# Kernel tuning notes

Measured on AMD Instinct MI355X. Metric: run time of the kernel, lower is better.

The kernel has to match this reference:

```python
import jax, jax.numpy as jnp
import numpy as np

H = 16        # query heads
HK = 8        # kv heads
D = 128       # head dim
HID = 2048    # hidden size
FF = 6144     # mlp intermediate
THETA = 1e6   # rope base (qwen3)
EPS = 1e-6
T = 2048      # total tokens


def rmsnorm(x, w):
    return x * jax.lax.rsqrt(jnp.mean(x * x, axis=-1, keepdims=True) + EPS) * w


def rope(pos, x):
    # x: [T, h, D], rotate-half RoPE
    half = D // 2
    inv = 1.0 / (THETA ** (jnp.arange(half, dtype=jnp.float32) / half))
    freqs = pos.astype(jnp.float32)[:, None] * inv          # [T, half]
    cos = jnp.cos(freqs)[:, None, :]
    sin = jnp.sin(freqs)[:, None, :]
    x1, x2 = x[..., :half], x[..., half:]
    return jnp.concatenate([x1 * cos - x2 * sin, x2 * cos + x1 * sin], axis=-1)


def setup_inputs() -> dict:
    key = jax.random.key(0)
    ks = jax.random.split(key, 12)
    s = 0.02
    return {
        "positions": jnp.arange(T, dtype=jnp.int32),
        "hidden_states": jax.random.normal(ks[0], (T, HID), dtype=jnp.float32),
        "wq": jax.random.normal(ks[1], (H * D, HID), dtype=jnp.float32) * s,
        "wk": jax.random.normal(ks[2], (HK * D, HID), dtype=jnp.float32) * s,
        "wv": jax.random.normal(ks[3], (HK * D, HID), dtype=jnp.float32) * s,
        "wo": jax.random.normal(ks[4], (HID, H * D), dtype=jnp.float32) * s,
        "q_norm_w": jnp.ones((D,), dtype=jnp.float32),
        "k_norm_w": jnp.ones((D,), dtype=jnp.float32),
        "ln1_w": jnp.ones((HID,), dtype=jnp.float32),
        "ln2_w": jnp.ones((HID,), dtype=jnp.float32),
        "w_gate": jax.random.normal(ks[5], (FF, HID), dtype=jnp.float32) * s,
        "w_up": jax.random.normal(ks[6], (FF, HID), dtype=jnp.float32) * s,
        "w_down": jax.random.normal(ks[7], (HID, FF), dtype=jnp.float32) * s,
    }


def reference(positions, hidden_states, wq, wk, wv, wo, q_norm_w, k_norm_w,
              ln1_w, ln2_w, w_gate, w_up, w_down):
    t = hidden_states.shape[0]
    residual = hidden_states
    h = rmsnorm(hidden_states, ln1_w)
    q = (h @ wq.T).reshape(t, H, D)
    k = (h @ wk.T).reshape(t, HK, D)
    v = (h @ wv.T).reshape(t, HK, D)
    q = rmsnorm(q, q_norm_w)
    k = rmsnorm(k, k_norm_w)
    q = rope(positions, q)
    k = rope(positions, k)
    # GQA: expand kv heads to query heads
    g = H // HK
    kr = jnp.repeat(k, g, axis=1)  # [t, H, D]
    vr = jnp.repeat(v, g, axis=1)
    scores = jnp.einsum('thd,shd->hts', q, kr) * (D ** -0.5)
    causal = positions[:, None] >= positions[None, :]
    scores = jnp.where(causal[None], scores, jnp.finfo(scores.dtype).min)
    p = jax.nn.softmax(scores, axis=-1)
    o = jnp.einsum('hts,shd->thd', p, vr).reshape(t, H * D)
    h = residual + o @ wo.T
    residual = h
    h = rmsnorm(h, ln2_w)
    h = (jax.nn.silu(h @ w_gate.T) * (h @ w_up.T)) @ w_down.T
    return residual + h
```

## Files before the change

kernel.cpp:

```cpp
#include <hip/hip_runtime.h>
#include <hip/hip_bf16.h>
#include <stdint.h>

namespace {

constexpr int kT   = 2048;
constexpr int kHid = 2048;
constexpr int kH   = 16;
constexpr int kHK  = 8;
constexpr int kD   = 128;
constexpr int kFF  = 6144;

using bf16x8 = __attribute__((ext_vector_type(8))) short;
using f32x4  = __attribute__((ext_vector_type(4))) float;

__device__ __forceinline__ float bf2f(unsigned short u) {
    return __uint_as_float(((unsigned)u) << 16);
}
__device__ __forceinline__ unsigned short f2bf(float f) {
    unsigned u = __float_as_uint(f);
    return (unsigned short)((u + 0x7fffu + ((u >> 16) & 1u)) >> 16);
}
__device__ __forceinline__ void gload_lds16(const void* g, void* l) {
    __builtin_amdgcn_global_load_lds(
        (__attribute__((address_space(1))) void*)g,
        (__attribute__((address_space(3))) void*)l, 16, 0, 0);
}
__device__ __forceinline__ f32x4 mf(bf16x8 a, bf16x8 b, f32x4 c) {
    return __builtin_amdgcn_mfma_f32_16x16x32_bf16(a, b, c, 0, 0, 0);
}

__global__ __launch_bounds__(256)
void cvt_f32_bf16(const float* __restrict__ src, unsigned short* __restrict__ dst, int n4) {
    int i = blockIdx.x * 256 + threadIdx.x;
    if (i < n4) {
        float4 v = ((const float4*)src)[i];
        ushort4 o;
        o.x = f2bf(v.x); o.y = f2bf(v.y); o.z = f2bf(v.z); o.w = f2bf(v.w);
        ((ushort4*)dst)[i] = o;
    }
}

__global__ __launch_bounds__(256)
void reduce4(const float* __restrict__ p0, const float* __restrict__ p1,
             const float* __restrict__ p2, const float* __restrict__ p3,
             const float* __restrict__ res, float* __restrict__ out, int n4) {
    int i = blockIdx.x * 256 + threadIdx.x;
    if (i < n4) {
        float4 a = ((const float4*)p0)[i];
        float4 b = ((const float4*)p1)[i];
        float4 c = ((const float4*)p2)[i];
        float4 d = ((const float4*)p3)[i];
        float4 r = ((const float4*)res)[i];
        float4 o;
        o.x = a.x + b.x + c.x + d.x + r.x;
        o.y = a.y + b.y + c.y + d.y + r.y;
        o.z = a.z + b.z + c.z + d.z + r.z;
        o.w = a.w + b.w + c.w + d.w + r.w;
        ((float4*)out)[i] = o;
    }
}

__global__ __launch_bounds__(256)
void rmsnorm_k(const float* __restrict__ x, const float* __restrict__ w,
               unsigned short* __restrict__ out) {
    const int row = blockIdx.x;
    const int tid = threadIdx.x;
    const float4* xr = (const float4*)(x + (size_t)row * kHid);
    float4 v0 = xr[tid];
    float4 v1 = xr[tid + 256];
    float ss = v0.x*v0.x + v0.y*v0.y + v0.z*v0.z + v0.w*v0.w
             + v1.x*v1.x + v1.y*v1.y + v1.z*v1.z + v1.w*v1.w;
#pragma unroll
    for (int m = 1; m < 64; m <<= 1) ss += __shfl_xor(ss, m);
    __shared__ float red[4];
    if ((tid & 63) == 0) red[tid >> 6] = ss;
    __syncthreads();
    float tot = red[0] + red[1] + red[2] + red[3];
    float rs = rsqrtf(tot * (1.0f / kHid) + 1e-6f);
    const float4* wv = (const float4*)w;
    float4 w0 = wv[tid], w1 = wv[tid + 256];
    ushort4 o0, o1;
    o0.x = f2bf(v0.x * rs * w0.x); o0.y = f2bf(v0.y * rs * w0.y);
    o0.z = f2bf(v0.z * rs * w0.z); o0.w = f2bf(v0.w * rs * w0.w);
    o1.x = f2bf(v1.x * rs * w1.x); o1.y = f2bf(v1.y * rs * w1.y);
    o1.z = f2bf(v1.z * rs * w1.z); o1.w = f2bf(v1.w * rs * w1.w);
    ushort4* orow = (ushort4*)(out + (size_t)row * kHid);
    orow[tid] = o0;
    orow[tid + 256] = o1;
}

__global__ __launch_bounds__(256)
void rmsnorm_red4(const float* __restrict__ p0, const float* __restrict__ p1,
                  const float* __restrict__ p2, const float* __restrict__ p3,
                  const float* __restrict__ res, const float* __restrict__ w,
                  float* __restrict__ H, unsigned short* __restrict__ out) {
    const int row = blockIdx.x;
    const int tid = threadIdx.x;
    const size_t base = (size_t)row * kHid;
    float4 v0, v1;
    {
        const float4* a = (const float4*)(p0 + base);
        const float4* b = (const float4*)(p1 + base);
        const float4* c = (const float4*)(p2 + base);
        const float4* d = (const float4*)(p3 + base);
        const float4* r = (const float4*)(res + base);
        float4 a0 = a[tid], b0 = b[tid], c0 = c[tid], d0 = d[tid], r0 = r[tid];
        v0.x = a0.x + b0.x + c0.x + d0.x + r0.x;
        v0.y = a0.y + b0.y + c0.y + d0.y + r0.y;
        v0.z = a0.z + b0.z + c0.z + d0.z + r0.z;
        v0.w = a0.w + b0.w + c0.w + d0.w + r0.w;
        float4 a1 = a[tid + 256], b1 = b[tid + 256], c1 = c[tid + 256],
               d1 = d[tid + 256], r1 = r[tid + 256];
        v1.x = a1.x + b1.x + c1.x + d1.x + r1.x;
        v1.y = a1.y + b1.y + c1.y + d1.y + r1.y;
        v1.z = a1.z + b1.z + c1.z + d1.z + r1.z;
        v1.w = a1.w + b1.w + c1.w + d1.w + r1.w;
    }
    ((float4*)(H + base))[tid] = v0;
    ((float4*)(H + base))[tid + 256] = v1;
    float ss = v0.x*v0.x + v0.y*v0.y + v0.z*v0.z + v0.w*v0.w
             + v1.x*v1.x + v1.y*v1.y + v1.z*v1.z + v1.w*v1.w;
#pragma unroll
    for (int m = 1; m < 64; m <<= 1) ss += __shfl_xor(ss, m);
    __shared__ float red[4];
    if ((tid & 63) == 0) red[tid >> 6] = ss;
    __syncthreads();
    float tot = red[0] + red[1] + red[2] + red[3];
    float rs = rsqrtf(tot * (1.0f / kHid) + 1e-6f);
    const float4* wv = (const float4*)w;
    float4 w0 = wv[tid], w1 = wv[tid + 256];
    ushort4 o0, o1;
    o0.x = f2bf(v0.x * rs * w0.x); o0.y = f2bf(v0.y * rs * w0.y);
    o0.z = f2bf(v0.z * rs * w0.z); o0.w = f2bf(v0.w * rs * w0.w);
    o1.x = f2bf(v1.x * rs * w1.x); o1.y = f2bf(v1.y * rs * w1.y);
    o1.z = f2bf(v1.z * rs * w1.z); o1.w = f2bf(v1.w * rs * w1.w);
    ushort4* orow = (ushort4*)(out + base);
    orow[tid] = o0;
    orow[tid + 256] = o1;
}

template <int EPI>
__global__ __launch_bounds__(512, 2)
void gemm256(const unsigned short* __restrict__ A,
             const unsigned short* __restrict__ B,
             void* __restrict__ C,
             int M, int N, int K, int KS,
             float* __restrict__ p0, float* __restrict__ p1,
             float* __restrict__ p2, float* __restrict__ p3) {
    __shared__ unsigned short smem[2][4][128 * 64];

    const int tid  = threadIdx.x;
    const int lane = tid & 63;
    const int l15  = lane & 15;
    const int g4   = lane >> 4;
    const int wid  = tid >> 6;
    const int wr   = wid >> 2;
    const int wc   = wid & 3;
    const int bm   = blockIdx.y * 256;
    const int bn   = blockIdx.x * 256;
    const int kb   = (EPI == 4) ? blockIdx.z * KS : 0;
    const int NT   = ((EPI == 4) ? KS : K) >> 6;
    const int NI   = NT >> 1;

    f32x4 acc[8][4] = {};

    auto stage = [&](int b, int reg, int t) {
        const unsigned short* Base = (reg < 2) ? A : B;
        const int br = ((reg < 2) ? bm : bn) + (reg & 1) * 128;
#pragma unroll
        for (int i = 0; i < 2; ++i) {
            int ch   = tid + i * 512;
            int row  = ch >> 3;
            int slot = (ch & 7) ^ (row & 7);
            gload_lds16(Base + (size_t)(br + row) * K + kb + t * 64 + slot * 8,
                        (char*)&smem[b][reg][0] + ch * 16);
        }
    };
    auto rdA = [&](int b, int m, int ks) {
        int row = m * 16 + l15;
        return *(const bf16x8*)((const char*)&smem[b][wr][0]
               + row * 128 + (((ks * 4 + g4) ^ (row & 7)) * 16));
    };
    auto rdB = [&](int b, int n, int ks) {
        int row = wc * 64 + n * 16 + l15;
        return *(const bf16x8*)((const char*)&smem[b][2 + (row >> 7)][0]
               + (row & 127) * 128 + (((ks * 4 + g4) ^ (row & 7)) * 16));
    };

    stage(0, 2, 0); stage(0, 3, 0); stage(0, 0, 0); stage(0, 1, 0);
    stage(1, 2, 1); stage(1, 3, 1); stage(1, 0, 1);
    asm volatile("s_waitcnt vmcnt(6)" ::: "memory");
    __builtin_amdgcn_s_barrier();

    for (int i = 0; i < NI; ++i) {
        const int e  = 2 * i;
        const int o  = e + 1;
        const bool pf = (e + 2 < NT);
        bf16x8 af[4][2], bfr[4][2];

#pragma unroll
        for (int m = 0; m < 4; ++m) { af[m][0] = rdA(0, m, 0); af[m][1] = rdA(0, m, 1); }
#pragma unroll
        for (int n = 0; n < 4; ++n) { bfr[n][0] = rdB(0, n, 0); bfr[n][1] = rdB(0, n, 1); }
        stage(1, 1, o);
        __builtin_amdgcn_s_barrier();
        asm volatile("s_waitcnt lgkmcnt(0)" ::: "memory");
        __builtin_amdgcn_sched_barrier(0);
        __builtin_amdgcn_s_setprio(1);
#pragma unroll
        for (int m = 0; m < 4; ++m)
#pragma unroll
            for (int n = 0; n < 2; ++n) {
                acc[m][n] = mf(af[m][0], bfr[n][0], acc[m][n]);
                acc[m][n] = mf(af[m][1], bfr[n][1], acc[m][n]);
            }
        __builtin_amdgcn_s_setprio(0);
        __builtin_amdgcn_s_barrier();

        if (pf) stage(0, 2, e + 2);
        __builtin_amdgcn_s_barrier();
        __builtin_amdgcn_s_setprio(1);
#pragma unroll
        for (int m = 0; m < 4; ++m)
#pragma unroll
            for (int n = 2; n < 4; ++n) {
                acc[m][n] = mf(af[m][0], bfr[n][0], acc[m][n]);
                acc[m][n] = mf(af[m][1], bfr[n][1], acc[m][n]);
            }
        __builtin_amdgcn_s_setprio(0);
        __builtin_amdgcn_s_barrier();

#pragma unroll
        for (int m = 0; m < 4; ++m) { af[m][0] = rdA(0, 4 + m, 0); af[m][1] = rdA(0, 4 + m, 1); }
        if (pf) stage(0, 3, e + 2);
        __builtin_amdgcn_s_barrier();
        asm volatile("s_waitcnt lgkmcnt(0)" ::: "memory");
        __builtin_amdgcn_sched_barrier(0);
        __builtin_amdgcn_s_setprio(1);
#pragma unroll
        for (int m = 0; m < 4; ++m)
#pragma unroll
            for (int n = 0; n < 2; ++n) {
                acc[4 + m][n] = mf(af[m][0], bfr[n][0], acc[4 + m][n]);
                acc[4 + m][n] = mf(af[m][1], bfr[n][1], acc[4 + m][n]);
            }
        __builtin_amdgcn_s_setprio(0);
        __builtin_amdgcn_s_barrier();

        if (pf) stage(0, 0, e + 2);
        __builtin_amdgcn_s_barrier();
        __builtin_amdgcn_s_setprio(1);
#pragma unroll
        for (int m = 0; m < 4; ++m)
#pragma unroll
            for (int n = 2; n < 4; ++n) {
                acc[4 + m][n] = mf(af[m][0], bfr[n][0], acc[4 + m][n]);
                acc[4 + m][n] = mf(af[m][1], bfr[n][1], acc[4 + m][n]);
            }
        __builtin_amdgcn_s_setprio(0);
        if (pf) asm volatile("s_waitcnt vmcnt(6)" ::: "memory");
        else    asm volatile("s_waitcnt vmcnt(0)" ::: "memory");
        __builtin_amdgcn_s_barrier();

#pragma unroll
        for (int m = 0; m < 4; ++m) { af[m][0] = rdA(1, m, 0); af[m][1] = rdA(1, m, 1); }
#pragma unroll
        for (int n = 0; n < 4; ++n) { bfr[n][0] = rdB(1, n, 0); bfr[n][1] = rdB(1, n, 1); }
        if (pf) stage(0, 1, e + 2);
        __builtin_amdgcn_s_barrier();
        asm volatile("s_waitcnt lgkmcnt(0)" ::: "memory");
        __builtin_amdgcn_sched_barrier(0);
        __builtin_amdgcn_s_setprio(1);
#pragma unroll
        for (int m = 0; m < 4; ++m)
#pragma unroll
            for (int n = 0; n < 2; ++n) {
                acc[m][n] = mf(af[m][0], bfr[n][0], acc[m][n]);
                acc[m][n] = mf(af[m][1], bfr[n][1], acc[m][n]);
            }
        __builtin_amdgcn_s_setprio(0);
        __builtin_amdgcn_s_barrier();

        if (pf) stage(1, 2, o + 2);
        __builtin_amdgcn_s_barrier();
        __builtin_amdgcn_s_setprio(1);
#pragma unroll
        for (int m = 0; m < 4; ++m)
#pragma unroll
            for (int n = 2; n < 4; ++n) {
                acc[m][n] = mf(af[m][0], bfr[n][0], acc[m][n]);
                acc[m][n] = mf(af[m][1], bfr[n][1], acc[m][n]);
            }
        __builtin_amdgcn_s_setprio(0);
        __builtin_amdgcn_s_barrier();

#pragma unroll
        for (int m = 0; m < 4; ++m) { af[m][0] = rdA(1, 4 + m, 0); af[m][1] = rdA(1, 4 + m, 1); }
        if (pf) stage(1, 3, o + 2);
        __builtin_amdgcn_s_barrier();
        asm volatile("s_waitcnt lgkmcnt(0)" ::: "memory");
        __builtin_amdgcn_sched_barrier(0);
        __builtin_amdgcn_s_setprio(1);
#pragma unroll
        for (int m = 0; m < 4; ++m)
#pragma unroll
            for (int n = 0; n < 2; ++n) {
                acc[4 + m][n] = mf(af[m][0], bfr[n][0], acc[4 + m][n]);
                acc[4 + m][n] = mf(af[m][1], bfr[n][1], acc[4 + m][n]);
            }
        __builtin_amdgcn_s_setprio(0);
        __builtin_amdgcn_s_barrier();

        if (pf) stage(1, 0, o + 2);
        __builtin_amdgcn_s_barrier();
        __builtin_amdgcn_s_setprio(1);
#pragma unroll
        for (int m = 0; m < 4; ++m)
#pragma unroll
            for (int n = 2; n < 4; ++n) {
                acc[4 + m][n] = mf(af[m][0], bfr[n][0], acc[4 + m][n]);
                acc[4 + m][n] = mf(af[m][1], bfr[n][1], acc[4 + m][n]);
            }
        __builtin_amdgcn_s_setprio(0);
        if (pf) asm volatile("s_waitcnt vmcnt(6)" ::: "memory");
        __builtin_amdgcn_s_barrier();
    }

    float* P = nullptr;
    if (EPI == 4) {
        const int z = blockIdx.z;
        P = (z == 0) ? p0 : (z == 1) ? p1 : (z == 2) ? p2 : p3;
    }
#pragma unroll
    for (int m = 0; m < 8; ++m) {
#pragma unroll
        for (int n = 0; n < 4; ++n) {
            int row = bm + wr * 128 + m * 16 + g4 * 4;
            int col = bn + wc * 64 + n * 16 + l15;
#pragma unroll
            for (int r = 0; r < 4; ++r) {
                size_t idx = (size_t)(row + r) * N + col;
                float v = acc[m][n][r];
                if (EPI == 0) ((float*)C)[idx] = v;
                else          P[idx] = v;
            }
        }
    }
}

template <int EPI>
__global__ __launch_bounds__(512, 2)
void gemm128(const unsigned short* __restrict__ A,
             const unsigned short* __restrict__ B,
             void* __restrict__ C,
             int M, int N, int K, int KS,
             float* __restrict__ p0, float* __restrict__ p1) {
    __shared__ unsigned short smem[2][3][128 * 64];

    const int tid  = threadIdx.x;
    const int lane = tid & 63;
    const int l15  = lane & 15;
    const int g4   = lane >> 4;
    const int wid  = tid >> 6;
    const int wr   = wid >> 2;
    const int wc   = wid & 3;
    const int bm   = blockIdx.y * 128;
    const int bn   = blockIdx.x * 256;
    const int kb   = (EPI == 4) ? blockIdx.z * KS : 0;
    const int NT   = ((EPI == 4) ? KS : K) >> 6;
    const int NI   = NT >> 1;

    f32x4 acc[4][4] = {};

    auto stage = [&](int b, int reg, int t) {
        const unsigned short* Base = (reg == 0) ? A : B;
        const int br = (reg == 0) ? bm : bn + (reg - 1) * 128;
#pragma unroll
        for (int i = 0; i < 2; ++i) {
            int ch   = tid + i * 512;
            int row  = ch >> 3;
            int slot = (ch & 7) ^ (row & 7);
            gload_lds16(Base + (size_t)(br + row) * K + kb + t * 64 + slot * 8,
                        (char*)&smem[b][reg][0] + ch * 16);
        }
    };
    auto rdA = [&](int b, int m, int ks) {
        int row = wr * 64 + m * 16 + l15;
        return *(const bf16x8*)((const char*)&smem[b][0][0]
               + row * 128 + (((ks * 4 + g4) ^ (row & 7)) * 16));
    };
    auto rdB = [&](int b, int n, int ks) {
        int row = wc * 64 + n * 16 + l15;
        return *(const bf16x8*)((const char*)&smem[b][1 + (row >> 7)][0]
               + (row & 127) * 128 + (((ks * 4 + g4) ^ (row & 7)) * 16));
    };

    stage(0, 1, 0); stage(0, 2, 0); stage(0, 0, 0);
    stage(1, 1, 1); stage(1, 2, 1);
    asm volatile("s_waitcnt vmcnt(4)" ::: "memory");
    __builtin_amdgcn_s_barrier();

    for (int i = 0; i < NI; ++i) {
        const int e  = 2 * i;
        const int o  = e + 1;
        const bool pf = (e + 2 < NT);
        bf16x8 af[4][2], bfr[4][2];

#pragma unroll
        for (int m = 0; m < 4; ++m) { af[m][0] = rdA(0, m, 0); af[m][1] = rdA(0, m, 1); }
#pragma unroll
        for (int n = 0; n < 4; ++n) { bfr[n][0] = rdB(0, n, 0); bfr[n][1] = rdB(0, n, 1); }
        stage(1, 0, o);
        __builtin_amdgcn_s_barrier();
        asm volatile("s_waitcnt lgkmcnt(0)" ::: "memory");
        __builtin_amdgcn_sched_barrier(0);
        __builtin_amdgcn_s_setprio(1);
#pragma unroll
        for (int m = 0; m < 4; ++m) {
            acc[m][0] = mf(af[m][0], bfr[0][0], acc[m][0]);
            acc[m][0] = mf(af[m][1], bfr[0][1], acc[m][0]);
        }
        __builtin_amdgcn_s_setprio(0);
        __builtin_amdgcn_s_barrier();

        if (pf) stage(0, 1, e + 2);
        __builtin_amdgcn_s_barrier();
        __builtin_amdgcn_s_setprio(1);
#pragma unroll
        for (int m = 0; m < 4; ++m) {
            acc[m][1] = mf(af[m][0], bfr[1][0], acc[m][1]);
            acc[m][1] = mf(af[m][1], bfr[1][1], acc[m][1]);
        }
        __builtin_amdgcn_s_setprio(0);
        __builtin_amdgcn_s_barrier();

        if (pf) stage(0, 2, e + 2);
        __builtin_amdgcn_s_barrier();
        __builtin_amdgcn_s_setprio(1);
#pragma unroll
        for (int m = 0; m < 4; ++m) {
            acc[m][2] = mf(af[m][0], bfr[2][0], acc[m][2]);
            acc[m][2] = mf(af[m][1], bfr[2][1], acc[m][2]);
        }
        __builtin_amdgcn_s_setprio(0);
        __builtin_amdgcn_s_barrier();

        __builtin_amdgcn_s_setprio(1);
#pragma unroll
        for (int m = 0; m < 4; ++m) {
            acc[m][3] = mf(af[m][0], bfr[3][0], acc[m][3]);
            acc[m][3] = mf(af[m][1], bfr[3][1], acc[m][3]);
        }
        __builtin_amdgcn_s_setprio(0);
        if (pf) asm volatile("s_waitcnt vmcnt(4)" ::: "memory");
        else    asm volatile("s_waitcnt vmcnt(0)" ::: "memory");
        __builtin_amdgcn_s_barrier();

#pragma unroll
        for (int m = 0; m < 4; ++m) { af[m][0] = rdA(1, m, 0); af[m][1] = rdA(1, m, 1); }
#pragma unroll
        for (int n = 0; n < 4; ++n) { bfr[n][0] = rdB(1, n, 0); bfr[n][1] = rdB(1, n, 1); }
        if (pf) stage(0, 0, e + 2);
        __builtin_amdgcn_s_barrier();
        asm volatile("s_waitcnt lgkmcnt(0)" ::: "memory");
        __builtin_amdgcn_sched_barrier(0);
        __builtin_amdgcn_s_setprio(1);
#pragma unroll
        for (int m = 0; m < 4; ++m) {
            acc[m][0] = mf(af[m][0], bfr[0][0], acc[m][0]);
            acc[m][0] = mf(af[m][1], bfr[0][1], acc[m][0]);
        }
        __builtin_amdgcn_s_setprio(0);
        __builtin_amdgcn_s_barrier();

        if (pf) stage(1, 1, o + 2);
        __builtin_amdgcn_s_barrier();
        __builtin_amdgcn_s_setprio(1);
#pragma unroll
        for (int m = 0; m < 4; ++m) {
            acc[m][1] = mf(af[m][0], bfr[1][0], acc[m][1]);
            acc[m][1] = mf(af[m][1], bfr[1][1], acc[m][1]);
        }
        __builtin_amdgcn_s_setprio(0);
        __builtin_amdgcn_s_barrier();

        if (pf) stage(1, 2, o + 2);
        __builtin_amdgcn_s_barrier();
        __builtin_amdgcn_s_setprio(1);
#pragma unroll
        for (int m = 0; m < 4; ++m) {
            acc[m][2] = mf(af[m][0], bfr[2][0], acc[m][2]);
            acc[m][2] = mf(af[m][1], bfr[2][1], acc[m][2]);
        }
        __builtin_amdgcn_s_setprio(0);
        __builtin_amdgcn_s_barrier();

        __builtin_amdgcn_s_setprio(1);
#pragma unroll
        for (int m = 0; m < 4; ++m) {
            acc[m][3] = mf(af[m][0], bfr[3][0], acc[m][3]);
            acc[m][3] = mf(af[m][1], bfr[3][1], acc[m][3]);
        }
        __builtin_amdgcn_s_setprio(0);
        if (pf) asm volatile("s_waitcnt vmcnt(4)" ::: "memory");
        __builtin_amdgcn_s_barrier();
    }

    float* P = nullptr;
    if (EPI == 4) P = (blockIdx.z == 0) ? p0 : p1;
#pragma unroll
    for (int m = 0; m < 4; ++m) {
#pragma unroll
        for (int n = 0; n < 4; ++n) {
            int row = bm + wr * 64 + m * 16 + g4 * 4;
            int col = bn + wc * 64 + n * 16 + l15;
#pragma unroll
            for (int r = 0; r < 4; ++r) {
                size_t idx = (size_t)(row + r) * N + col;
                float v = acc[m][n][r];
                if (EPI == 0) ((float*)C)[idx] = v;
                else          P[idx] = v;
            }
        }
    }
}

__global__ __launch_bounds__(512, 2)
void gemm_gu(const unsigned short* __restrict__ A,
             const unsigned short* __restrict__ WGp,
             const unsigned short* __restrict__ WUp,
             unsigned short* __restrict__ OUT) {
    __shared__ unsigned short smem[2][28672];

    const int tid  = threadIdx.x;
    const int lane = tid & 63;
    const int l15  = lane & 15;
    const int g4   = lane >> 4;
    const int wid  = tid >> 6;
    const int wr   = wid >> 1;
    const int wc   = wid & 1;
    const int bm   = blockIdx.y * 256;
    const int bn   = blockIdx.x * 96;
    const int K    = kHid;
    const int NT   = K >> 6;
    const int NI   = NT >> 1;

    f32x4 accg[4][3] = {};
    f32x4 accu[4][3] = {};

    constexpr int OFF_A0 = 0;
    constexpr int OFF_A1 = 16384;
    constexpr int OFF_GU = 32768;

    auto stage_a = [&](int b, int half, int t) {
#pragma unroll
        for (int i = 0; i < 2; ++i) {
            int ch   = tid + i * 512;
            int row  = ch >> 3;
            int slot = (ch & 7) ^ (row & 7);
            gload_lds16(A + (size_t)(bm + half * 128 + row) * K + t * 64 + slot * 8,
                        (char*)&smem[b][0] + (half ? OFF_A1 : OFF_A0) + ch * 16);
        }
    };
    auto stage_gu = [&](int b, int t) {
#pragma unroll
        for (int i = 0; i < 3; ++i) {
            int ch   = tid + i * 512;
            int row  = ch >> 3;
            int slot = (ch & 7) ^ (row & 7);
            const unsigned short* Base = (row >= 96) ? WUp : WGp;
            int srow = bn + (row >= 96 ? row - 96 : row);
            gload_lds16(Base + (size_t)srow * K + t * 64 + slot * 8,
                        (char*)&smem[b][0] + OFF_GU + ch * 16);
        }
    };
    auto rdA = [&](int b, int m, int ks) {
        int rt  = wr * 64 + m * 16 + l15;
        int row = rt & 127;
        return *(const bf16x8*)((const char*)&smem[b][0]
               + (rt >> 7 ? OFF_A1 : OFF_A0)
               + row * 128 + (((ks * 4 + g4) ^ (row & 7)) * 16));
    };
    auto rdG = [&](int b, int n, int ks) {
        int row = wc * 48 + n * 16 + l15;
        return *(const bf16x8*)((const char*)&smem[b][0] + OFF_GU
               + row * 128 + (((ks * 4 + g4) ^ (row & 7)) * 16));
    };
    auto rdU = [&](int b, int n, int ks) {
        int row = 96 + wc * 48 + n * 16 + l15;
        return *(const bf16x8*)((const char*)&smem[b][0] + OFF_GU
               + row * 128 + (((ks * 4 + g4) ^ (row & 7)) * 16));
    };

    stage_a(0, 0, 0); stage_a(0, 1, 0); stage_gu(0, 0);
    stage_a(1, 0, 1); stage_a(1, 1, 1);
    asm volatile("s_waitcnt vmcnt(4)" ::: "memory");
    __builtin_amdgcn_s_barrier();

    for (int i = 0; i < NI; ++i) {
        const int e  = 2 * i;
        const int o  = e + 1;
        const bool pf = (e + 2 < NT);
        bf16x8 af[4][2], bg[3][2], bu[3][2];

#pragma unroll
        for (int m = 0; m < 4; ++m) { af[m][0] = rdA(0, m, 0); af[m][1] = rdA(0, m, 1); }
#pragma unroll
        for (int n = 0; n < 3; ++n) { bg[n][0] = rdG(0, n, 0); bg[n][1] = rdG(0, n, 1); }
        stage_gu(1, o);
        __builtin_amdgcn_s_barrier();
        asm volatile("s_waitcnt lgkmcnt(0)" ::: "memory");
        __builtin_amdgcn_sched_barrier(0);
        __builtin_amdgcn_s_setprio(1);
#pragma unroll
        for (int m = 0; m < 4; ++m)
#pragma unroll
            for (int n = 0; n < 3; ++n)
                accg[m][n] = mf(af[m][0], bg[n][0], accg[m][n]);
        __builtin_amdgcn_s_setprio(0);
        __builtin_amdgcn_s_barrier();

        if (pf) stage_a(0, 0, e + 2);
        __builtin_amdgcn_s_barrier();
        __builtin_amdgcn_s_setprio(1);
#pragma unroll
        for (int m = 0; m < 4; ++m)
#pragma unroll
            for (int n = 0; n < 3; ++n)
                accg[m][n] = mf(af[m][1], bg[n][1], accg[m][n]);
        __builtin_amdgcn_s_setprio(0);
        __builtin_amdgcn_s_barrier();

#pragma unroll
        for (int n = 0; n < 3; ++n) { bu[n][0] = rdU(0, n, 0); bu[n][1] = rdU(0, n, 1); }
        if (pf) stage_a(0, 1, e + 2);
        __builtin_amdgcn_s_barrier();
        asm volatile("s_waitcnt lgkmcnt(0)" ::: "memory");
        __builtin_amdgcn_sched_barrier(0);
        __builtin_amdgcn_s_setprio(1);
#pragma unroll
        for (int m = 0; m < 4; ++m)
#pragma unroll
            for (int n = 0; n < 3; ++n)
                accu[m][n] = mf(af[m][0], bu[n][0], accu[m][n]);
        __builtin_amdgcn_s_setprio(0);
        __builtin_amdgcn_s_barrier();

        if (pf) stage_gu(0, e + 2);
        __builtin_amdgcn_s_barrier();
        __builtin_amdgcn_s_setprio(1);
#pragma unroll
        for (int m = 0; m < 4; ++m)
#pragma unroll
            for (int n = 0; n < 3; ++n)
                accu[m][n] = mf(af[m][1], bu[n][1], accu[m][n]);
        __builtin_amdgcn_s_setprio(0);
        if (pf) asm volatile("s_waitcnt vmcnt(7)" ::: "memory");
        else    asm volatile("s_waitcnt vmcnt(0)" ::: "memory");
        __builtin_amdgcn_s_barrier();

#pragma unroll
        for (int m = 0; m < 4; ++m) { af[m][0] = rdA(1, m, 0); af[m][1] = rdA(1, m, 1); }
#pragma unroll
        for (int n = 0; n < 3; ++n) { bg[n][0] = rdG(1, n, 0); bg[n][1] = rdG(1, n, 1); }
        __builtin_amdgcn_s_barrier();
        asm volatile("s_waitcnt lgkmcnt(0)" ::: "memory");
        __builtin_amdgcn_sched_barrier(0);
        __builtin_amdgcn_s_setprio(1);
#pragma unroll
        for (int m = 0; m < 4; ++m)
#pragma unroll
            for (int n = 0; n < 3; ++n)
                accg[m][n] = mf(af[m][0], bg[n][0], accg[m][n]);
        __builtin_amdgcn_s_setprio(0);
        __builtin_amdgcn_s_barrier();

        if (pf) stage_a(1, 0, o + 2);
        __builtin_amdgcn_s_barrier();
        __builtin_amdgcn_s_setprio(1);
#pragma unroll
        for (int m = 0; m < 4; ++m)
#pragma unroll
            for (int n = 0; n < 3; ++n)
                accg[m][n] = mf(af[m][1], bg[n][1], accg[m][n]);
        __builtin_amdgcn_s_setprio(0);
        __builtin_amdgcn_s_barrier();

#pragma unroll
        for (int n = 0; n < 3; ++n) { bu[n][0] = rdU(1, n, 0); bu[n][1] = rdU(1, n, 1); }
        if (pf) stage_a(1, 1, o + 2);
        __builtin_amdgcn_s_barrier();
        asm volatile("s_waitcnt lgkmcnt(0)" ::: "memory");
        __builtin_amdgcn_sched_barrier(0);
        __builtin_amdgcn_s_setprio(1);
#pragma unroll
        for (int m = 0; m < 4; ++m)
#pragma unroll
            for (int n = 0; n < 3; ++n)
                accu[m][n] = mf(af[m][0], bu[n][0], accu[m][n]);
        __builtin_amdgcn_s_setprio(0);
        __builtin_amdgcn_s_barrier();

        __builtin_amdgcn_s_setprio(1);
#pragma unroll
        for (int m = 0; m < 4; ++m)
#pragma unroll
            for (int n = 0; n < 3; ++n)
                accu[m][n] = mf(af[m][1], bu[n][1], accu[m][n]);
        __builtin_amdgcn_s_setprio(0);
        if (pf) asm volatile("s_waitcnt vmcnt(4)" ::: "memory");
        __builtin_amdgcn_s_barrier();
    }

#pragma unroll
    for (int m = 0; m < 4; ++m) {
#pragma unroll
        for (int n = 0; n < 3; ++n) {
            int row = bm + wr * 64 + m * 16 + g4 * 4;
            int col = bn + wc * 48 + n * 16 + l15;
#pragma unroll
            for (int r = 0; r < 4; ++r) {
                float g = accg[m][n][r];
                float u = accu[m][n][r];
                OUT[(size_t)(row + r) * kFF + col] = f2bf(g / (1.0f + __expf(-g)) * u);
            }
        }
    }
}

__global__ __launch_bounds__(256)
void qknorm_rope(const float* __restrict__ qkv, const int* __restrict__ positions,
                 const float* __restrict__ qnw, const float* __restrict__ knw,
                 unsigned short* __restrict__ Qo, unsigned short* __restrict__ Ko) {
    const int t    = blockIdx.x;
    const int j    = blockIdx.y * 4 + (threadIdx.x >> 6);
    const int lane = threadIdx.x & 63;
    const float* src = qkv + (size_t)t * 4096 + j * 128;
    float x1 = src[lane];
    float x2 = src[lane + 64];
    float ss = x1 * x1 + x2 * x2;
#pragma unroll
    for (int m = 1; m < 64; m <<= 1) ss += __shfl_xor(ss, m);
    float rs = rsqrtf(ss * (1.0f / 128.0f) + 1e-6f);
    const float* w = (j < 16) ? qnw : knw;
    float n1 = x1 * rs * w[lane];
    float n2 = x2 * rs * w[lane + 64];
    float inv = powf(1.0e6f, -(float)lane * (1.0f / 64.0f));
    float fr = (float)positions[t] * inv;
    float sn, cs;
    sincosf(fr, &sn, &cs);
    float o1 = n1 * cs - n2 * sn;
    float o2 = n2 * cs + n1 * sn;
    if (j < 16) {
        unsigned short* d = Qo + (size_t)t * (kH * kD) + j * kD;
        d[lane] = f2bf(o1);
        d[lane + 64] = f2bf(o2);
    } else {
        unsigned short* d = Ko + (size_t)t * (kHK * kD) + (j - 16) * kD;
        d[lane] = f2bf(o1);
        d[lane + 64] = f2bf(o2);
    }
}

__global__ __launch_bounds__(256)
void vtrans(const float* __restrict__ qkv, unsigned short* __restrict__ Vt) {
    __shared__ float tile[32][33];
    const int t0 = blockIdx.x * 32;
    const int d0 = blockIdx.y * 32;
    const int tc = threadIdx.x & 31;
    const int tr = threadIdx.x >> 5;
#pragma unroll
    for (int i = 0; i < 4; ++i) {
        int trow = tr + i * 8;
        tile[trow][tc] = qkv[(size_t)(t0 + trow) * 4096 + 3072 + d0 + tc];
    }
    __syncthreads();
#pragma unroll
    for (int i = 0; i < 4; ++i) {
        int drow = tr + i * 8;
        Vt[(size_t)(d0 + drow) * kT + t0 + tc] = f2bf(tile[tc][drow]);
    }
}

__global__ __launch_bounds__(512, 4)
void attn_fwd5(const unsigned short* __restrict__ Q,
               const unsigned short* __restrict__ Kc,
               const unsigned short* __restrict__ Vt,
               unsigned short* __restrict__ O) {
    __shared__ unsigned short Kb[2][64 * 128];
    __shared__ unsigned short Vb[2][128 * 64];
    __shared__ float MergeML[4][2][64];

    const int tid  = threadIdx.x;
    const int lane = tid & 63;
    const int l15  = lane & 15;
    const int g4   = lane >> 4;
    const int wid  = tid >> 6;
    const int s    = wid & 1;
    const int grp  = wid >> 1;
    const int hs   = grp >> 1;
    const int qsub = grp & 1;
    const int hkk  = blockIdx.x;
    const int h    = hkk * 2 + hs;
    const int nby  = gridDim.y;
    const int by   = blockIdx.y;
    const int byl  = (by & 1) ? (nby - 1 - (by >> 1)) : (by >> 1);
    const int q0   = byl * 32 + qsub * 16;
    const int nch  = byl / 2 + 1;
    const int c0   = (nch + 1) >> 1;
    const int myn  = s ? (nch - c0) : c0;
    const int qi   = q0 + l15;
    const int vt   = grp * 64 + lane;

    const int addrA = ((g4 & 1) * 32 + l15) * 4;
    const int addrB = addrA + 64;
    const int addrQ = g4 * 80;
    const bool hb   = (g4 >> 1) != 0;

    bf16x8 qf[4];
#pragma unroll
    for (int ks = 0; ks < 4; ++ks)
        qf[ks] = *(const bf16x8*)(Q + (size_t)(q0 + l15) * (kH * kD) + h * kD + ks * 32 + g4 * 8);

    f32x4 oacc[8] = {};
    float mrun = -3e38f, lrun = 0.f;
    const float scale = 0.08838834764831845f;

    auto stage = [&](int kv0) {
#pragma unroll
        for (int i = 0; i < 4; ++i) {
            int ch  = vt + i * 256;
            int row = ch >> 4;
            int c16 = ch & 15;
            gload_lds16(Kc + (size_t)(kv0 + row) * (kHK * kD) + hkk * kD
                            + ((c16 ^ (row & 7)) * 8),
                        (char*)Kb[s] + ch * 16);
        }
#pragma unroll
        for (int i = 0; i < 4; ++i) {
            int ch  = vt + i * 256;
            int row = ch >> 3;
            int c8  = ch & 7;
            gload_lds16(Vt + (size_t)(hkk * kD + row) * kT + kv0
                            + ((c8 ^ (row & 7)) * 8),
                        (char*)Vb[s] + ch * 16);
        }
    };

    for (int c = 0; c < c0; ++c) {
        const bool act = c < myn;
        const int kv0 = (s ? (c0 + c) : c) * 64;
        if (act) stage(kv0);
        asm volatile("s_waitcnt vmcnt(0)" ::: "memory");
        __builtin_amdgcn_s_barrier();
        __builtin_amdgcn_sched_barrier(0);

        if (act) {
            f32x4 sa[4] = {};
            __builtin_amdgcn_s_setprio(1);
#pragma unroll
            for (int hh = 0; hh < 4; ++hh) {
                const int row = hh * 16 + l15;
#pragma unroll
                for (int ks = 0; ks < 4; ++ks) {
                    bf16x8 kf = *(const bf16x8*)((const char*)Kb[s]
                                  + row * 256 + (((ks * 4 + g4) ^ (row & 7)) * 16));
                    sa[hh] = mf(kf, qf[ks], sa[hh]);
                }
            }
            __builtin_amdgcn_s_setprio(0);

            float sv[4][4];
#pragma unroll
            for (int hh = 0; hh < 4; ++hh)
#pragma unroll
                for (int r = 0; r < 4; ++r)
                    sv[hh][r] = sa[hh][r] * scale;
            if (kv0 + 63 > q0) {
#pragma unroll
                for (int hh = 0; hh < 4; ++hh)
#pragma unroll
                    for (int r = 0; r < 4; ++r) {
                        int ki = kv0 + hh * 16 + g4 * 4 + r;
                        if (ki > qi) sv[hh][r] = -3e38f;
                    }
            }

            float m16;
            {
                float a = fmaxf(fmaxf(sv[0][0], sv[0][1]), fmaxf(sv[0][2], sv[0][3]));
                float b2 = fmaxf(fmaxf(sv[1][0], sv[1][1]), fmaxf(sv[1][2], sv[1][3]));
                float c2 = fmaxf(fmaxf(sv[2][0], sv[2][1]), fmaxf(sv[2][2], sv[2][3]));
                float d2 = fmaxf(fmaxf(sv[3][0], sv[3][1]), fmaxf(sv[3][2], sv[3][3]));
                m16 = fmaxf(fmaxf(a, b2), fmaxf(c2, d2));
            }
            m16 = fmaxf(m16, __shfl_xor(m16, 16));
            m16 = fmaxf(m16, __shfl_xor(m16, 32));

            if (__any(m16 > mrun)) {
                float mnew = fmaxf(mrun, m16);
                float corr = __expf(mrun - mnew);
                mrun = mnew;
                lrun *= corr;
                float cr[4];
#pragma unroll
                for (int r = 0; r < 4; ++r)
                    cr[r] = __int_as_float(__builtin_amdgcn_ds_bpermute(
                                addrQ + 4 * r, __float_as_int(corr)));
#pragma unroll
                for (int c2 = 0; c2 < 8; ++c2)
#pragma unroll
                    for (int r = 0; r < 4; ++r)
                        oacc[c2][r] *= cr[r];
            }

            float p[4][4];
            float ps = 0.f;
#pragma unroll
            for (int hh = 0; hh < 4; ++hh)
#pragma unroll
                for (int r = 0; r < 4; ++r) {
                    float pe = __expf(sv[hh][r] - mrun);
                    p[hh][r] = pe;
                    ps += pe;
                }
            ps += __shfl_xor(ps, 16);
            ps += __shfl_xor(ps, 32);
            lrun += ps;

            unsigned pk[4][2];
#pragma unroll
            for (int hh = 0; hh < 4; ++hh) {
                asm("v_cvt_pk_bf16_f32 %0, %1, %2"
                    : "=v"(pk[hh][0]) : "v"(p[hh][0]), "v"(p[hh][1]));
                asm("v_cvt_pk_bf16_f32 %0, %1, %2"
                    : "=v"(pk[hh][1]) : "v"(p[hh][2]), "v"(p[hh][3]));
            }
            int ex[4][2][2];
#pragma unroll
            for (int hh = 0; hh < 4; ++hh)
#pragma unroll
                for (int ii = 0; ii < 2; ++ii) {
                    ex[hh][ii][0] = __builtin_amdgcn_ds_bpermute(addrA, (int)pk[hh][ii]);
                    ex[hh][ii][1] = __builtin_amdgcn_ds_bpermute(addrB, (int)pk[hh][ii]);
                }
            union { int w[4]; bf16x8 v; } pu0, pu1;
#pragma unroll
            for (int jw = 0; jw < 4; ++jw) {
                pu0.w[jw] = hb ? ex[1][jw & 1][jw >> 1] : ex[0][jw & 1][jw >> 1];
                pu1.w[jw] = hb ? ex[3][jw & 1][jw >> 1] : ex[2][jw & 1][jw >> 1];
            }
            bf16x8 pa0 = pu0.v;
            bf16x8 pa1 = pu1.v;

            __builtin_amdgcn_s_setprio(1);
#pragma unroll
            for (int c2 = 0; c2 < 8; ++c2) {
                const int d = c2 * 16 + l15;
                bf16x8 vf0 = *(const bf16x8*)((const char*)Vb[s]
                              + d * 128 + ((g4 ^ (d & 7)) * 16));
                oacc[c2] = mf(pa0, vf0, oacc[c2]);
                bf16x8 vf1 = *(const bf16x8*)((const char*)Vb[s]
                              + d * 128 + ((((4 + g4) ^ (d & 7))) * 16));
                oacc[c2] = mf(pa1, vf1, oacc[c2]);
            }
            __builtin_amdgcn_s_setprio(0);
        }
        __builtin_amdgcn_s_barrier();
    }

    float* KbF = (float*)&Kb[0][0];
    if (s == 1) {
        MergeML[grp][0][lane] = mrun;
        MergeML[grp][1][lane] = lrun;
#pragma unroll
        for (int c2 = 0; c2 < 8; ++c2)
#pragma unroll
            for (int r = 0; r < 4; ++r)
                KbF[grp * 2048 + (c2 * 4 + r) * 64 + lane] = oacc[c2][r];
    }
    asm volatile("s_waitcnt lgkmcnt(0)" ::: "memory");
    __builtin_amdgcn_s_barrier();

    if (s == 0) {
        float m1 = MergeML[grp][0][lane];
        float l1 = MergeML[grp][1][lane];
        float mg = fmaxf(mrun, m1);
        float a0 = __expf(mrun - mg);
        float a1 = __expf(m1 - mg);
        float L  = lrun * a0 + l1 * a1;
        float ar0[4], ar1[4], Lr[4];
#pragma unroll
        for (int r = 0; r < 4; ++r) {
            ar0[r] = __int_as_float(__builtin_amdgcn_ds_bpermute(
                         addrQ + 4 * r, __float_as_int(a0)));
            ar1[r] = __int_as_float(__builtin_amdgcn_ds_bpermute(
                         addrQ + 4 * r, __float_as_int(a1)));
            Lr[r]  = __int_as_float(__builtin_amdgcn_ds_bpermute(
                         addrQ + 4 * r, __float_as_int(L)));
        }
#pragma unroll
        for (int c2 = 0; c2 < 8; ++c2)
#pragma unroll
            for (int r = 0; r < 4; ++r) {
                float oex = KbF[grp * 2048 + (c2 * 4 + r) * 64 + lane];
                float v = (oacc[c2][r] * ar0[r] + oex * ar1[r]) / Lr[r];
                O[(size_t)(q0 + g4 * 4 + r) * (kH * kD) + h * kD + c2 * 16 + l15] = f2bf(v);
            }
    }
}

}

extern "C" void kernel_launch(void* const* d_in, const int* in_sizes, int n_in,
                              void* d_out, int out_size, void* d_ws, size_t ws_size,
                              hipStream_t stream) {
    (void)in_sizes; (void)n_in; (void)out_size; (void)ws_size;

    const int*   positions = (const int*)  d_in[0];
    const float* hidden    = (const float*)d_in[1];
    const float* wq  = (const float*)d_in[2];
    const float* wk  = (const float*)d_in[3];
    const float* wv  = (const float*)d_in[4];
    const float* wo  = (const float*)d_in[5];
    const float* qnw = (const float*)d_in[6];
    const float* knw = (const float*)d_in[7];
    const float* ln1 = (const float*)d_in[8];
    const float* ln2 = (const float*)d_in[9];
    const float* wg  = (const float*)d_in[10];
    const float* wu  = (const float*)d_in[11];
    const float* wd  = (const float*)d_in[12];

    char* ws = (char*)d_ws;
    unsigned short* WQKV = (unsigned short*)(ws + 0);
    unsigned short* WO   = (unsigned short*)(ws + 16777216);
    unsigned short* WG   = (unsigned short*)(ws + 25165824);
    unsigned short* WU   = (unsigned short*)(ws + 50331648);
    unsigned short* WD   = (unsigned short*)(ws + 75497472);
    unsigned short* XN1  = (unsigned short*)(ws + 100663296);
    unsigned short* OATT = (unsigned short*)(ws + 109051904);
    float*          H1   = (float*)(ws + 117440512);
    unsigned short* XN2  = (unsigned short*)(ws + 134217728);
    float*          QKVF = (float*)(ws + 142606336);
    unsigned short* QB   = (unsigned short*)(ws + 176160768);
    unsigned short* KB   = (unsigned short*)(ws + 184549376);
    unsigned short* VT   = (unsigned short*)(ws + 188743680);
    unsigned short* ACT  = (unsigned short*)(ws + 167772160);

    float* OP0 = (float*)(ws + 142606336);
    float* OP1 = (float*)(ws + 159383552);
    float* OP2 = (float*)(ws + 176160768);
    float* OP3 = (float*)(ws + 0);
    float* DP0 = (float*)(ws + 0);
    float* DP1 = (float*)(ws + 16777216);
    float* DP2 = (float*)(ws + 33554432);
    float* DP3 = (float*)(ws + 142606336);

    auto cvt = [&](const float* s, unsigned short* dst, size_t n) {
        int n4 = (int)(n / 4);
        cvt_f32_bf16<<<dim3((n4 + 255) / 256), dim3(256), 0, stream>>>(s, dst, n4);
    };

    cvt(wq, WQKV,                 (size_t)kH  * kD * kHid);
    cvt(wk, WQKV + 2048 * kHid,   (size_t)kHK * kD * kHid);
    cvt(wv, WQKV + 3072 * kHid,   (size_t)kHK * kD * kHid);
    cvt(wo, WO,                   (size_t)kHid * kH * kD);
    cvt(wg, WG,                   (size_t)kFF * kHid);
    cvt(wu, WU,                   (size_t)kFF * kHid);
    cvt(wd, WD,                   (size_t)kHid * kFF);

    rmsnorm_k<<<dim3(kT), dim3(256), 0, stream>>>(hidden, ln1, XN1);

    gemm128<0><<<dim3(4096 / 256, kT / 128), dim3(512), 0, stream>>>(
        XN1, WQKV, QKVF, kT, 4096, kHid, kHid, nullptr, nullptr);

    qknorm_rope<<<dim3(kT, 6), dim3(256), 0, stream>>>(QKVF, positions, qnw, knw, QB, KB);
    vtrans<<<dim3(kT / 32, 1024 / 32), dim3(256), 0, stream>>>(QKVF, VT);

    attn_fwd5<<<dim3(kHK, kT / 32), dim3(512), 0, stream>>>(QB, KB, VT, OATT);

    gemm256<4><<<dim3(kHid / 256, kT / 256, 4), dim3(512), 0, stream>>>(
        OATT, WO, nullptr, kT, kHid, kHid, 512, OP0, OP1, OP2, OP3);
    rmsnorm_red4<<<dim3(kT), dim3(256), 0, stream>>>(
        OP0, OP1, OP2, OP3, hidden, ln2, H1, XN2);

    gemm_gu<<<dim3(kFF / 96, kT / 256), dim3(512), 0, stream>>>(XN2, WG, WU, ACT);

    gemm256<4><<<dim3(kHid / 256, kT / 256, 4), dim3(512), 0, stream>>>(
        ACT, WD, nullptr, kT, kHid, kFF, 1536, DP0, DP1, DP2, DP3);
    reduce4<<<dim3(kT * kHid / 4 / 256), dim3(256), 0, stream>>>(
        DP0, DP1, DP2, DP3, H1, (float*)d_out, kT * kHid / 4);
}
```

Baseline: 386.3 us.

## Double-buffer K tiles in LDS and load V fragments directly from global

The attention kernel now prefetches the next K tile into a second LDS buffer while computing on the current one, waiting on only the older loads. V tiles no longer go through LDS: each lane loads its V fragments straight from global memory into registers at the start of each chunk. This is meant to overlap K loading with compute and to remove LDS traffic and bank pressure for V. In exchange it uses more VGPRs for the V fragments and makes V loads uncoalesced per-lane global reads whose latency may be exposed before the PV MFMAs.

New measurement: 589.5 us. 1.53x slower.

```diff
diff --git a/kernel.cpp b/kernel.cpp
--- a/kernel.cpp
+++ b/kernel.cpp
@@ -784,12 +784,11 @@
 }
 
 __global__ __launch_bounds__(512, 4)
-void attn_fwd5(const unsigned short* __restrict__ Q,
+void attn_fwd6(const unsigned short* __restrict__ Q,
                const unsigned short* __restrict__ Kc,
                const unsigned short* __restrict__ Vt,
                unsigned short* __restrict__ O) {
-    __shared__ unsigned short Kb[2][64 * 128];
-    __shared__ unsigned short Vb[2][128 * 64];
+    __shared__ unsigned short Kb[2][2][64 * 128];
     __shared__ float MergeML[4][2][64];
 
     const int tid  = threadIdx.x;
@@ -823,11 +822,16 @@
     for (int ks = 0; ks < 4; ++ks)
         qf[ks] = *(const bf16x8*)(Q + (size_t)(q0 + l15) * (kH * kD) + h * kD + ks * 32 + g4 * 8);
 
+    const unsigned short* vbase[8];
+#pragma unroll
+    for (int c2 = 0; c2 < 8; ++c2)
+        vbase[c2] = Vt + (size_t)(hkk * kD + c2 * 16 + l15) * kT + g4 * 8;
+
     f32x4 oacc[8] = {};
     float mrun = -3e38f, lrun = 0.f;
     const float scale = 0.08838834764831845f;
 
-    auto stage = [&](int kv0) {
+    auto stage_k = [&](int b, int kv0) {
 #pragma unroll
         for (int i = 0; i < 4; ++i) {
             int ch  = vt + i * 256;
@@ -835,28 +839,30 @@
             int c16 = ch & 15;
             gload_lds16(Kc + (size_t)(kv0 + row) * (kHK * kD) + hkk * kD
                             + ((c16 ^ (row & 7)) * 8),
-                        (char*)Kb[s] + ch * 16);
-        }
-#pragma unroll
-        for (int i = 0; i < 4; ++i) {
-            int ch  = vt + i * 256;
-            int row = ch >> 3;
-            int c8  = ch & 7;
-            gload_lds16(Vt + (size_t)(hkk * kD + row) * kT + kv0
-                            + ((c8 ^ (row & 7)) * 8),
-                        (char*)Vb[s] + ch * 16);
-        }
-    };
+                        (char*)Kb[s][b] + ch * 16);
+        }
+    };
+
+    if (myn > 0) stage_k(0, (s ? c0 : 0) * 64);
 
     for (int c = 0; c < c0; ++c) {
-        const bool act = c < myn;
-        const int kv0 = (s ? (c0 + c) : c) * 64;
-        if (act) stage(kv0);
-        asm volatile("s_waitcnt vmcnt(0)" ::: "memory");
+        const bool act  = c < myn;
+        const bool actn = (c + 1) < myn;
+        const int  b    = c & 1;
+        const int  kv0  = ((s ? c0 : 0) + c) * 64;
+        if (actn) stage_k(b ^ 1, kv0 + 64);
+        asm volatile("s_waitcnt vmcnt(4)" ::: "memory");
         __builtin_amdgcn_s_barrier();
         __builtin_amdgcn_sched_barrier(0);
 
         if (act) {
+            bf16x8 vf0[8], vf1[8];
+#pragma unroll
+            for (int c2 = 0; c2 < 8; ++c2) {
+                vf0[c2] = *(const bf16x8*)(vbase[c2] + kv0);
+                vf1[c2] = *(const bf16x8*)(vbase[c2] + kv0 + 32);
+            }
+
             f32x4 sa[4] = {};
             __builtin_amdgcn_s_setprio(1);
 #pragma unroll
@@ -864,7 +870,7 @@
                 const int row = hh * 16 + l15;
 #pragma unroll
                 for (int ks = 0; ks < 4; ++ks) {
-                    bf16x8 kf = *(const bf16x8*)((const char*)Kb[s]
+                    bf16x8 kf = *(const bf16x8*)((const char*)Kb[s][b]
                                   + row * 256 + (((ks * 4 + g4) ^ (row & 7)) * 16));
                     sa[hh] = mf(kf, qf[ks], sa[hh]);
                 }
@@ -957,20 +963,15 @@
             __builtin_amdgcn_s_setprio(1);
 #pragma unroll
             for (int c2 = 0; c2 < 8; ++c2) {
-                const int d = c2 * 16 + l15;
-                bf16x8 vf0 = *(const bf16x8*)((const char*)Vb[s]
-                              + d * 128 + ((g4 ^ (d & 7)) * 16));
-                oacc[c2] = mf(pa0, vf0, oacc[c2]);
-                bf16x8 vf1 = *(const bf16x8*)((const char*)Vb[s]
-                              + d * 128 + ((((4 + g4) ^ (d & 7))) * 16));
-                oacc[c2] = mf(pa1, vf1, oacc[c2]);
+                oacc[c2] = mf(pa0, vf0[c2], oacc[c2]);
+                oacc[c2] = mf(pa1, vf1[c2], oacc[c2]);
             }
             __builtin_amdgcn_s_setprio(0);
         }
         __builtin_amdgcn_s_barrier();
     }
 
-    float* KbF = (float*)&Kb[0][0];
+    float* KbF = (float*)&Kb[0][0][0];
     if (s == 1) {
         MergeML[grp][0][lane] = mrun;
         MergeML[grp][1][lane] = lrun;
@@ -1078,7 +1079,7 @@
     qknorm_rope<<<dim3(kT, 6), dim3(256), 0, stream>>>(QKVF, positions, qnw, knw, QB, KB);
     vtrans<<<dim3(kT / 32, 1024 / 32), dim3(256), 0, stream>>>(QKVF, VT);
 
-    attn_fwd5<<<dim3(kHK, kT / 32), dim3(512), 0, stream>>>(QB, KB, VT, OATT);
+    attn_fwd6<<<dim3(kHK, kT / 32), dim3(512), 0, stream>>>(QB, KB, VT, OATT);
 
     gemm256<4><<<dim3(kHid / 256, kT / 256, 4), dim3(512), 0, stream>>>(
         OATT, WO, nullptr, kT, kHid, kHid, 512, OP0, OP1, OP2, OP3);
```

## Prefetch next K tile into registers to overlap loads with attention compute

Applied to the files above, without the earlier changes.

The attention kernel now splits K and V staging. The next chunk's K tile is loaded into registers while the current chunk's QK^T and softmax run, then written to LDS after a barrier. V for the current chunk is still loaded directly to LDS, with finer vmcnt waits so the V load overlaps the score computation. This is meant to hide global load latency that was exposed by the old full vmcnt(0) wait at the start of every chunk, at the cost of extra VGPRs, an extra barrier and an LDS store per iteration.

Result: no change. 391.9 us (+1.5%).

```diff
diff --git a/kernel.cpp b/kernel.cpp
--- a/kernel.cpp
+++ b/kernel.cpp
@@ -784,7 +784,7 @@
 }
 
 __global__ __launch_bounds__(512, 4)
-void attn_fwd5(const unsigned short* __restrict__ Q,
+void attn_fwd7(const unsigned short* __restrict__ Q,
                const unsigned short* __restrict__ Kc,
                const unsigned short* __restrict__ Vt,
                unsigned short* __restrict__ O) {
@@ -812,6 +812,7 @@
     const int myn  = s ? (nch - c0) : c0;
     const int qi   = q0 + l15;
     const int vt   = grp * 64 + lane;
+    const int base = s ? c0 : 0;
 
     const int addrA = ((g4 & 1) * 32 + l15) * 4;
     const int addrB = addrA + 64;
@@ -827,7 +828,7 @@
     float mrun = -3e38f, lrun = 0.f;
     const float scale = 0.08838834764831845f;
 
-    auto stage = [&](int kv0) {
+    auto stage_k_lds = [&](int kv0) {
 #pragma unroll
         for (int i = 0; i < 4; ++i) {
             int ch  = vt + i * 256;
@@ -837,6 +838,8 @@
                             + ((c16 ^ (row & 7)) * 8),
                         (char*)Kb[s] + ch * 16);
         }
+    };
+    auto stage_v = [&](int kv0) {
 #pragma unroll
         for (int i = 0; i < 4; ++i) {
             int ch  = vt + i * 256;
@@ -848,14 +851,40 @@
         }
     };
 
+    if (myn > 0) stage_k_lds(base * 64);
+
     for (int c = 0; c < c0; ++c) {
-        const bool act = c < myn;
-        const int kv0 = (s ? (c0 + c) : c) * 64;
-        if (act) stage(kv0);
-        asm volatile("s_waitcnt vmcnt(0)" ::: "memory");
-        __builtin_amdgcn_s_barrier();
-        __builtin_amdgcn_sched_barrier(0);
-
+        const bool act  = c < myn;
+        const bool actn = (c + 1) < myn;
+        const int  kv0  = (base + c) * 64;
+
+        if (act) stage_v(kv0);
+        __builtin_amdgcn_sched_barrier(0);
+        bf16x8 kreg0, kreg1, kreg2, kreg3;
+        if (actn) {
+            const int kvn = kv0 + 64;
+#define LD_K(i, dst)                                                          \
+            {                                                                 \
+                int ch  = vt + (i) * 256;                                     \
+                int row = ch >> 4;                                            \
+                int c16 = ch & 15;                                            \
+                dst = *(const bf16x8*)(Kc + (size_t)(kvn + row) * (kHK * kD)  \
+                          + hkk * kD + ((c16 ^ (row & 7)) * 8));              \
+            }
+            LD_K(0, kreg0) LD_K(1, kreg1) LD_K(2, kreg2) LD_K(3, kreg3)
+#undef LD_K
+        }
+        __builtin_amdgcn_sched_barrier(0);
+        if (c == 0) {
+            if (act) {
+                if (actn) asm volatile("s_waitcnt vmcnt(8)" ::: "memory");
+                else      asm volatile("s_waitcnt vmcnt(4)" ::: "memory");
+            }
+            __builtin_amdgcn_s_barrier();
+            __builtin_amdgcn_sched_barrier(0);
+        }
+
+        bf16x8 pa0, pa1;
         if (act) {
             f32x4 sa[4] = {};
             __builtin_amdgcn_s_setprio(1);
@@ -951,9 +980,26 @@
                 pu0.w[jw] = hb ? ex[1][jw & 1][jw >> 1] : ex[0][jw & 1][jw >> 1];
                 pu1.w[jw] = hb ? ex[3][jw & 1][jw >> 1] : ex[2][jw & 1][jw >> 1];
             }
-            bf16x8 pa0 = pu0.v;
-            bf16x8 pa1 = pu1.v;
-
+            pa0 = pu0.v;
+            pa1 = pu1.v;
+
+            if (actn) asm volatile("s_waitcnt vmcnt(4)" ::: "memory");
+            else      asm volatile("s_waitcnt vmcnt(0)" ::: "memory");
+        }
+        __builtin_amdgcn_s_barrier();
+        __builtin_amdgcn_sched_barrier(0);
+
+        if (actn) {
+            asm volatile("s_waitcnt vmcnt(0)" ::: "memory");
+#pragma unroll
+            for (int i = 0; i < 4; ++i) {
+                int ch = vt + i * 256;
+                bf16x8 kv = (i == 0) ? kreg0 : (i == 1) ? kreg1 : (i == 2) ? kreg2 : kreg3;
+                *(bf16x8*)((char*)Kb[s] + ch * 16) = kv;
+            }
+        }
+
+        if (act) {
             __builtin_amdgcn_s_setprio(1);
 #pragma unroll
             for (int c2 = 0; c2 < 8; ++c2) {
@@ -967,6 +1013,7 @@
             }
             __builtin_amdgcn_s_setprio(0);
         }
+        asm volatile("s_waitcnt lgkmcnt(0)" ::: "memory");
         __builtin_amdgcn_s_barrier();
     }
 
@@ -1078,7 +1125,7 @@
     qknorm_rope<<<dim3(kT, 6), dim3(256), 0, stream>>>(QKVF, positions, qnw, knw, QB, KB);
     vtrans<<<dim3(kT / 32, 1024 / 32), dim3(256), 0, stream>>>(QKVF, VT);
 
-    attn_fwd5<<<dim3(kHK, kT / 32), dim3(512), 0, stream>>>(QB, KB, VT, OATT);
+    attn_fwd7<<<dim3(kHK, kT / 32), dim3(512), 0, stream>>>(QB, KB, VT, OATT);
 
     gemm256<4><<<dim3(kHid / 256, kT / 256, 4), dim3(512), 0, stream>>>(
         OATT, WO, nullptr, kT, kHid, kHid, 512, OP0, OP1, OP2, OP3);
```
